# Kernel tuning notes

Measured on AMD Instinct MI355X. Metric: run time of the kernel, lower is better.

## Reference

```python
import jax, jax.numpy as jnp
import numpy as np

N_NODES = 50000
N_EDGES = 25000
NNZ = 600000
D = 128
H = 256
DEPTH = 2


def setup_inputs() -> dict:
    key = jax.random.key(0)
    ks = jax.random.split(key, 12)
    x = jax.random.normal(ks[0], (N_NODES, D), dtype=jnp.float32)
    v_idx = jax.random.randint(ks[1], (NNZ,), 0, N_NODES)
    e_idx = jax.random.randint(ks[2], (NNZ,), 0, N_EDGES)
    s = 0.05
    W1 = jax.random.normal(ks[3], (H, D), dtype=jnp.float32) * s
    b1 = jnp.zeros((H,), jnp.float32)
    W2 = jax.random.normal(ks[4], (D, H), dtype=jnp.float32) * s
    b2 = jnp.zeros((D,), jnp.float32)
    Wu = jax.random.normal(ks[5], (D, D), dtype=jnp.float32) * s
    bu = jnp.zeros((D,), jnp.float32)
    Wa = jax.random.normal(ks[6], (4, D), dtype=jnp.float32) * s
    ba = jnp.zeros((4,), jnp.float32)
    return {"x": x, "v_idx": v_idx, "e_idx": e_idx, "W1": W1, "b1": b1,
            "W2": W2, "b2": b2, "Wu": Wu, "bu": bu, "Wa": Wa, "ba": ba}


def reference(x, v_idx, e_idx, W1, b1, W2, b2, Wu, bu, Wa, ba):
    ones = jnp.ones((v_idx.shape[0],), x.dtype)
    # degrees for mean aggregation (clamped to avoid div-by-zero)
    edeg = jnp.maximum(jax.ops.segment_sum(ones, e_idx, num_segments=N_EDGES), 1.0)
    vdeg = jnp.maximum(jax.ops.segment_sum(ones, v_idx, num_segments=N_NODES), 1.0)

    def v2v_mean(m):
        # vertex -> hyperedge (mean), then hyperedge -> vertex (mean)
        e_feat = jax.ops.segment_sum(m[v_idx], e_idx, num_segments=N_EDGES) / edeg[:, None]
        return jax.ops.segment_sum(e_feat[e_idx], v_idx, num_segments=N_NODES) / vdeg[:, None]

    def update(h):
        m = jax.nn.relu(h @ W1.T + b1)   # [N, H]
        m = jax.nn.relu(m @ W2.T + b2)   # [N, D]  (dropout = identity in eval)
        m_i = v2v_mean(m)                # [N, D]
        return jax.nn.relu(h @ Wu.T + bu + m_i)

    for _ in range(DEPTH):
        x = update(x)
    a = x @ Wa.T + ba                    # [N, 4]
    return jax.nn.log_softmax(a, axis=1)
```

## Files before the change

kernel.cpp:

```cpp
#include <hip/hip_runtime.h>
#include <hip/hip_bf16.h>
#include <math.h>

#define N_NODES 50000
#define N_EDGES 25000
#define NNZ     600000
#define D       128
#define H       256

#define BW    98
#define NBE   256
#define NBV   511
#define CAPE  3072
#define CAPV  1536
#define CHUNK 4096

typedef short short8 __attribute__((ext_vector_type(8)));
typedef float floatx4 __attribute__((ext_vector_type(4)));

__device__ inline ushort f2bf(float f) {
    uint u = __float_as_uint(f);
    u += 0x7FFF + ((u >> 16) & 1);
    return (ushort)(u >> 16);
}
__device__ inline float bflo(uint u) { return __uint_as_float(u << 16); }
__device__ inline float bfhi(uint u) { return __uint_as_float(u & 0xffff0000u); }

__global__ void convert_all(const float* __restrict__ x,  ushort* __restrict__ xb,
                            const float* __restrict__ W1, ushort* __restrict__ W1b,
                            const float* __restrict__ W2, ushort* __restrict__ W2b,
                            const float* __restrict__ Wu, ushort* __restrict__ Wub) {
    const int nx = N_NODES * D / 4;
    const int n1 = H * D / 4;
    const int n2 = D * H / 4;
    const int nu = D * D / 4;
    int i = blockIdx.x * blockDim.x + threadIdx.x;
    const float* src; ushort* dst; int j = i;
    if (j < nx)                { src = x;  dst = xb;  }
    else if ((j -= nx) < n1)   { src = W1; dst = W1b; }
    else if ((j -= n1) < n2)   { src = W2; dst = W2b; }
    else if ((j -= n2) < nu)   { src = Wu; dst = Wub; }
    else return;
    float4 v = ((const float4*)src)[j];
    ushort4 o;
    o.x = f2bf(v.x); o.y = f2bf(v.y); o.z = f2bf(v.z); o.w = f2bf(v.w);
    ((ushort4*)dst)[j] = o;
}

__global__ void bucket_place(const int* __restrict__ v_idx, const int* __restrict__ e_idx,
                             int* __restrict__ cntE, int* __restrict__ cntV,
                             int2* __restrict__ recE, int2* __restrict__ recV) {
    __shared__ int hE[NBE], hV[NBV];
    __shared__ int rE[NBE], rV[NBV];
    for (int i = threadIdx.x; i < NBE; i += 256) hE[i] = 0;
    for (int i = threadIdx.x; i < NBV; i += 256) hV[i] = 0;
    __syncthreads();
    int base = blockIdx.x * CHUNK;
    int end  = min(base + CHUNK, NNZ);
    int myE[16], myV[16];
    #pragma unroll
    for (int j = 0; j < 16; ++j) {
        int i = base + threadIdx.x + j * 256;
        myE[j] = -1; myV[j] = -1;
        if (i < end) {
            myE[j] = e_idx[i];
            myV[j] = v_idx[i];
            atomicAdd(&hE[myE[j] / BW], 1);
            atomicAdd(&hV[myV[j] / BW], 1);
        }
    }
    __syncthreads();
    for (int i = threadIdx.x; i < NBE; i += 256) {
        int c = hE[i];
        rE[i] = c ? atomicAdd(&cntE[i], c) : 0;
    }
    for (int i = threadIdx.x; i < NBV; i += 256) {
        int c = hV[i];
        rV[i] = c ? atomicAdd(&cntV[i], c) : 0;
    }
    __syncthreads();
    for (int i = threadIdx.x; i < NBE; i += 256) hE[i] = 0;
    for (int i = threadIdx.x; i < NBV; i += 256) hV[i] = 0;
    __syncthreads();
    #pragma unroll
    for (int j = 0; j < 16; ++j) {
        if (myE[j] >= 0) {
            int bk = myE[j] / BW;
            int p = rE[bk] + atomicAdd(&hE[bk], 1);
            recE[(size_t)bk * CAPE + p] = make_int2(myE[j], myV[j]);
            bk = myV[j] / BW;
            p = rV[bk] + atomicAdd(&hV[bk], 1);
            recV[(size_t)bk * CAPV + p] = make_int2(myV[j], myE[j]);
        }
    }
}

__global__ void bucket_final(const int2* __restrict__ recE, const int* __restrict__ cntE,
                             const int2* __restrict__ recV, const int* __restrict__ cntV,
                             int2* __restrict__ e_sd, float* __restrict__ erecip, int* __restrict__ e_vert,
                             int2* __restrict__ v_sd, float* __restrict__ vrecip, int* __restrict__ v_edge) {
    __shared__ int hist[BW], scn[BW], cur[BW];
    const bool eSide = blockIdx.x < NBE;
    const int b = eSide ? blockIdx.x : blockIdx.x - NBE;
    const int cap   = eSide ? CAPE : CAPV;
    const int2* rec = (eSide ? recE : recV) + (size_t)b * cap;
    const int cnt   = (eSide ? cntE : cntV)[b];
    const int nseg  = eSide ? N_EDGES : N_NODES;
    int2* sd        = eSide ? e_sd : v_sd;
    float* recip    = eSide ? erecip : vrecip;
    int* outv       = (eSide ? e_vert : v_edge) + (size_t)b * cap;
    const int k0 = b * BW;

    for (int i = threadIdx.x; i < BW; i += 256) hist[i] = 0;
    __syncthreads();
    for (int i = threadIdx.x; i < cnt; i += 256)
        atomicAdd(&hist[rec[i].x - k0], 1);
    __syncthreads();

    if (threadIdx.x < 64) {
        int lane = threadIdx.x;
        int v0 = hist[lane];
        int a = v0;
        #pragma unroll
        for (int d = 1; d < 64; d <<= 1) {
            int u = __shfl_up(a, d, 64);
            if (lane >= d) a += u;
        }
        scn[lane] = a - v0;
        int tot0 = __shfl(a, 63, 64);
        int v1 = (lane < BW - 64) ? hist[64 + lane] : 0;
        int a1 = v1;
        #pragma unroll
        for (int d = 1; d < 64; d <<= 1) {
            int u = __shfl_up(a1, d, 64);
            if (lane >= d) a1 += u;
        }
        if (lane < BW - 64) scn[64 + lane] = tot0 + a1 - v1;
    }
    __syncthreads();

    const int gbase = b * cap;
    for (int i = threadIdx.x; i < BW; i += 256) {
        int seg = k0 + i;
        if (seg < nseg) {
            sd[seg] = make_int2(gbase + scn[i], hist[i]);
            recip[seg] = 1.0f / (float)max(hist[i], 1);
        }
        cur[i] = scn[i];
    }
    __syncthreads();
    for (int i = threadIdx.x; i < cnt; i += 256) {
        int2 r = rec[i];
        int p = atomicAdd(&cur[r.x - k0], 1);
        outv[p] = r.y;
    }
}

__global__ void gather_rows(const ushort* __restrict__ src,
                            const int2* __restrict__ sd,
                            const int* __restrict__ list,
                            const float* __restrict__ recip,
                            const ushort* __restrict__ uadd,
                            ushort* __restrict__ outbuf,
                            const float* __restrict__ Wa,
                            const float* __restrict__ ba,
                            float* __restrict__ headout,
                            int nseg) {
    long long gtid = (long long)blockIdx.x * blockDim.x + threadIdx.x;
    int seg = (int)(gtid >> 4);
    int ql  = threadIdx.x & 15;
    if (seg >= nseg) return;
    int2 dsc = sd[seg];
    int s = dsc.x, cnt = dsc.y;
    const ushort* sp = src + ql * 8;

    float f0 = 0.f, f1 = 0.f, f2 = 0.f, f3 = 0.f;
    float f4 = 0.f, f5 = 0.f, f6 = 0.f, f7 = 0.f;

    int p = 0;
    for (; p + 4 <= cnt; p += 4) {
        int r0 = list[s + p + 0];
        int r1 = list[s + p + 1];
        int r2 = list[s + p + 2];
        int r3 = list[s + p + 3];
        uint4 t0 = *(const uint4*)(sp + (size_t)r0 * D);
        uint4 t1 = *(const uint4*)(sp + (size_t)r1 * D);
        uint4 t2 = *(const uint4*)(sp + (size_t)r2 * D);
        uint4 t3 = *(const uint4*)(sp + (size_t)r3 * D);
        f0 += bflo(t0.x) + bflo(t1.x) + bflo(t2.x) + bflo(t3.x);
        f1 += bfhi(t0.x) + bfhi(t1.x) + bfhi(t2.x) + bfhi(t3.x);
        f2 += bflo(t0.y) + bflo(t1.y) + bflo(t2.y) + bflo(t3.y);
        f3 += bfhi(t0.y) + bfhi(t1.y) + bfhi(t2.y) + bfhi(t3.y);
        f4 += bflo(t0.z) + bflo(t1.z) + bflo(t2.z) + bflo(t3.z);
        f5 += bfhi(t0.z) + bfhi(t1.z) + bfhi(t2.z) + bfhi(t3.z);
        f6 += bflo(t0.w) + bflo(t1.w) + bflo(t2.w) + bflo(t3.w);
        f7 += bfhi(t0.w) + bfhi(t1.w) + bfhi(t2.w) + bfhi(t3.w);
    }
    for (; p < cnt; ++p) {
        int r0 = list[s + p];
        uint4 t0 = *(const uint4*)(sp + (size_t)r0 * D);
        f0 += bflo(t0.x);  f1 += bfhi(t0.x);
        f2 += bflo(t0.y);  f3 += bfhi(t0.y);
        f4 += bflo(t0.z);  f5 += bfhi(t0.z);
        f6 += bflo(t0.w);  f7 += bfhi(t0.w);
    }

    float rc = recip[seg];
    f0 *= rc; f1 *= rc; f2 *= rc; f3 *= rc;
    f4 *= rc; f5 *= rc; f6 *= rc; f7 *= rc;
    if (uadd) {
        uint4 uv = *(const uint4*)(uadd + (size_t)seg * D + ql * 8);
        f0 = fmaxf(f0 + bflo(uv.x), 0.f);  f1 = fmaxf(f1 + bfhi(uv.x), 0.f);
        f2 = fmaxf(f2 + bflo(uv.y), 0.f);  f3 = fmaxf(f3 + bfhi(uv.y), 0.f);
        f4 = fmaxf(f4 + bflo(uv.z), 0.f);  f5 = fmaxf(f5 + bfhi(uv.z), 0.f);
        f6 = fmaxf(f6 + bflo(uv.w), 0.f);  f7 = fmaxf(f7 + bfhi(uv.w), 0.f);
    }
    if (headout) {
        float av[4];
        #pragma unroll
        for (int j = 0; j < 4; ++j) {
            const float* wr = Wa + j * D + ql * 8;
            float4 wA = *(const float4*)wr;
            float4 wB = *(const float4*)(wr + 4);
            float pj = f0 * wA.x + f1 * wA.y + f2 * wA.z + f3 * wA.w
                     + f4 * wB.x + f5 * wB.y + f6 * wB.z + f7 * wB.w;
            pj += __shfl_xor(pj, 1, 64);
            pj += __shfl_xor(pj, 2, 64);
            pj += __shfl_xor(pj, 4, 64);
            pj += __shfl_xor(pj, 8, 64);
            av[j] = pj + ba[j];
        }
        if (ql == 0) {
            float mx = fmaxf(fmaxf(av[0], av[1]), fmaxf(av[2], av[3]));
            float se = expf(av[0] - mx) + expf(av[1] - mx)
                     + expf(av[2] - mx) + expf(av[3] - mx);
            float lse = mx + logf(se);
            float4 o = make_float4(av[0] - lse, av[1] - lse, av[2] - lse, av[3] - lse);
            *(float4*)(headout + (size_t)seg * 4) = o;
        }
    } else {
        uint4 o;
        o.x = ((uint)f2bf(f1) << 16) | (uint)f2bf(f0);
        o.y = ((uint)f2bf(f3) << 16) | (uint)f2bf(f2);
        o.z = ((uint)f2bf(f5) << 16) | (uint)f2bf(f4);
        o.w = ((uint)f2bf(f7) << 16) | (uint)f2bf(f6);
        *(uint4*)(outbuf + (size_t)seg * D + ql * 8) = o;
    }
}

__launch_bounds__(256, 3)
__global__ void mlp_fused(const ushort* __restrict__ A,
                          const ushort* __restrict__ W1b,
                          const float* __restrict__ b1,
                          const ushort* __restrict__ W2b,
                          const float* __restrict__ b2,
                          const ushort* __restrict__ Wub,
                          const float* __restrict__ bu,
                          ushort* __restrict__ m2out,
                          ushort* __restrict__ uout,
                          int M) {
    __shared__ ushort Af[64][136];
    __shared__ __align__(16) char Pbuf[18432];
    __shared__ ushort m1c[64][72];
    ushort* P = (ushort*)Pbuf;
    float (*Cs)[68] = (float(*)[68])Pbuf;

    const int tid = threadIdx.x;
    const int w = tid >> 6, lane = tid & 63;
    const int quad = lane >> 4, mrow = lane & 15;
    const int rowBase = blockIdx.x * 64;
    const int orow = tid >> 2;
    const int c0   = (tid & 3) << 4;

    #pragma unroll
    for (int r = 0; r < 4; ++r) {
        int idx = tid + r * 256;
        int row = idx >> 4;
        int c   = (idx & 15) << 3;
        uint4 av = make_uint4(0, 0, 0, 0);
        if (rowBase + row < M)
            av = *(const uint4*)(A + (size_t)(rowBase + row) * D + c);
        *(uint4*)&Af[row][c] = av;
    }

    for (int n0 = 0; n0 < D; n0 += 64) {
        __syncthreads();
        #pragma unroll
        for (int r = 0; r < 4; ++r) {
            int idx = tid + r * 256;
            int row = idx >> 4;
            int c   = (idx & 15) << 3;
            *(uint4*)&P[row * 136 + c] = *(const uint4*)(Wub + (size_t)(n0 + row) * D + c);
        }
        __syncthreads();
        floatx4 acc[4] = {{0,0,0,0},{0,0,0,0},{0,0,0,0},{0,0,0,0}};
        #pragma unroll
        for (int k0 = 0; k0 < D; k0 += 32) {
            short8 af = *(const short8*)&Af[w * 16 + mrow][k0 + quad * 8];
            #pragma unroll
            for (int t = 0; t < 4; ++t) {
                short8 bfr = *(const short8*)&P[(t * 16 + mrow) * 136 + k0 + quad * 8];
                acc[t] = __builtin_amdgcn_mfma_f32_16x16x32_bf16(af, bfr, acc[t], 0, 0, 0);
            }
        }
        __syncthreads();
        #pragma unroll
        for (int t = 0; t < 4; ++t)
            #pragma unroll
            for (int r = 0; r < 4; ++r)
                Cs[w * 16 + quad * 4 + r][t * 16 + mrow] = acc[t][r];
        __syncthreads();
        if (rowBase + orow < M) {
            union { ushort u16[16]; uint4 u4[2]; } ov;
            #pragma unroll
            for (int j4 = 0; j4 < 4; ++j4) {
                float4 bb = *(const float4*)(bu + n0 + c0 + j4 * 4);
                float bjv[4] = {bb.x, bb.y, bb.z, bb.w};
                #pragma unroll
                for (int j = 0; j < 4; ++j)
                    ov.u16[j4 * 4 + j] = f2bf(Cs[orow][c0 + j4 * 4 + j] + bjv[j]);
            }
            ushort* cp = uout + (size_t)(rowBase + orow) * D + n0 + c0;
            *(uint4*)cp = ov.u4[0];
            *(uint4*)(cp + 8) = ov.u4[1];
        }
    }

    floatx4 acc2[8] = {{0,0,0,0},{0,0,0,0},{0,0,0,0},{0,0,0,0},
                       {0,0,0,0},{0,0,0,0},{0,0,0,0},{0,0,0,0}};
    for (int kc = 0; kc < 4; ++kc) {
        __syncthreads();
        #pragma unroll
        for (int r = 0; r < 4; ++r) {
            int idx = tid + r * 256;
            int row = idx >> 4;
            int c   = (idx & 15) << 3;
            *(uint4*)&P[row * 136 + c] = *(const uint4*)(W1b + (size_t)(kc * 64 + row) * D + c);
        }
        __syncthreads();
        floatx4 acc1[4] = {{0,0,0,0},{0,0,0,0},{0,0,0,0},{0,0,0,0}};
        #pragma unroll
        for (int k0 = 0; k0 < D; k0 += 32) {
            short8 af = *(const short8*)&Af[w * 16 + mrow][k0 + quad * 8];
            #pragma unroll
            for (int t = 0; t < 4; ++t) {
                short8 bfr = *(const short8*)&P[(t * 16 + mrow) * 136 + k0 + quad * 8];
                acc1[t] = __builtin_amdgcn_mfma_f32_16x16x32_bf16(af, bfr, acc1[t], 0, 0, 0);
            }
        }
        #pragma unroll
        for (int t = 0; t < 4; ++t) {
            float bb = b1[kc * 64 + t * 16 + mrow];
            #pragma unroll
            for (int r = 0; r < 4; ++r)
                m1c[w * 16 + quad * 4 + r][t * 16 + mrow] = f2bf(fmaxf(acc1[t][r] + bb, 0.f));
        }
        __syncthreads();
        #pragma unroll
        for (int r = 0; r < 4; ++r) {
            int idx = tid + r * 256;
            int row = idx >> 3;
            int c8  = (idx & 7) << 3;
            *(uint4*)&P[row * 72 + c8] = *(const uint4*)(W2b + (size_t)row * H + kc * 64 + c8);
        }
        __syncthreads();
        #pragma unroll
        for (int k0 = 0; k0 < 64; k0 += 32) {
            short8 af = *(const short8*)&m1c[w * 16 + mrow][k0 + quad * 8];
            #pragma unroll
            for (int t2 = 0; t2 < 8; ++t2) {
                short8 bfr = *(const short8*)&P[(t2 * 16 + mrow) * 72 + k0 + quad * 8];
                acc2[t2] = __builtin_amdgcn_mfma_f32_16x16x32_bf16(af, bfr, acc2[t2], 0, 0, 0);
            }
        }
    }

    #pragma unroll
    for (int hh = 0; hh < 2; ++hh) {
        __syncthreads();
        #pragma unroll
        for (int t = 0; t < 4; ++t)
            #pragma unroll
            for (int r = 0; r < 4; ++r)
                Cs[w * 16 + quad * 4 + r][t * 16 + mrow] = acc2[hh * 4 + t][r];
        __syncthreads();
        if (rowBase + orow < M) {
            union { ushort u16[16]; uint4 u4[2]; } ov;
            #pragma unroll
            for (int j4 = 0; j4 < 4; ++j4) {
                float4 bb = *(const float4*)(b2 + hh * 64 + c0 + j4 * 4);
                float bjv[4] = {bb.x, bb.y, bb.z, bb.w};
                #pragma unroll
                for (int j = 0; j < 4; ++j) {
                    float v = Cs[orow][c0 + j4 * 4 + j] + bjv[j];
                    ov.u16[j4 * 4 + j] = f2bf(fmaxf(v, 0.f));
                }
            }
            ushort* cp = m2out + (size_t)(rowBase + orow) * D + hh * 64 + c0;
            *(uint4*)cp = ov.u4[0];
            *(uint4*)(cp + 8) = ov.u4[1];
        }
    }
}

extern "C" void kernel_launch(void* const* d_in, const int* in_sizes, int n_in,
                              void* d_out, int out_size, void* d_ws, size_t ws_size,
                              hipStream_t stream) {
    const float* x     = (const float*)d_in[0];
    const int*   v_idx = (const int*)d_in[1];
    const int*   e_idx = (const int*)d_in[2];
    const float* W1    = (const float*)d_in[3];
    const float* b1    = (const float*)d_in[4];
    const float* W2    = (const float*)d_in[5];
    const float* b2    = (const float*)d_in[6];
    const float* Wu    = (const float*)d_in[7];
    const float* bu    = (const float*)d_in[8];
    const float* Wa    = (const float*)d_in[9];
    const float* ba    = (const float*)d_in[10];
    float* out = (float*)d_out;

    char* wsp = (char*)d_ws;
    auto alloc = [&](size_t bytes) -> char* {
        char* p = wsp;
        wsp += (bytes + 255) & ~(size_t)255;
        return p;
    };

    ushort* xb     = (ushort*)alloc((size_t)N_NODES * D * 2);
    ushort* hA     = (ushort*)alloc((size_t)N_NODES * D * 2);
    ushort* m2b    = (ushort*)alloc((size_t)N_NODES * D * 2);
    ushort* ub     = (ushort*)alloc((size_t)N_NODES * D * 2);
    ushort* e_feat = (ushort*)alloc((size_t)N_EDGES * D * 2);
    ushort* W1b    = (ushort*)alloc((size_t)H * D * 2);
    ushort* W2b    = (ushort*)alloc((size_t)D * H * 2);
    ushort* Wub    = (ushort*)alloc((size_t)D * D * 2);
    int*    e_vert = (int*)alloc((size_t)NBE * CAPE * 4);
    int*    v_edge = (int*)alloc((size_t)NBV * CAPV * 4);
    int2*   recE   = (int2*)alloc((size_t)NBE * CAPE * 8);
    int2*   recV   = (int2*)alloc((size_t)NBV * CAPV * 8);
    int*    cntE   = (int*)alloc((size_t)(NBE + NBV) * 4);
    int*    cntV   = cntE + NBE;
    int2*   e_sd   = (int2*)alloc((size_t)N_EDGES * 8);
    int2*   v_sd   = (int2*)alloc((size_t)N_NODES * 8);
    float*  erecip = (float*)alloc((size_t)N_EDGES * 4);
    float*  vrecip = (float*)alloc((size_t)N_NODES * 4);

    const int cooBlocks = (NNZ + CHUNK - 1) / CHUNK;
    const int convTotal = N_NODES * D / 4 + H * D / 4 + D * H / 4 + D * D / 4;

    convert_all<<<(convTotal + 255) / 256, 256, 0, stream>>>(
        x, xb, W1, W1b, W2, W2b, Wu, Wub);

    hipMemsetAsync(cntE, 0, (size_t)(NBE + NBV) * 4, stream);
    bucket_place<<<cooBlocks, 256, 0, stream>>>(v_idx, e_idx, cntE, cntV, recE, recV);
    bucket_final<<<NBE + NBV, 256, 0, stream>>>(recE, cntE, recV, cntV,
                                                e_sd, erecip, e_vert,
                                                v_sd, vrecip, v_edge);

    const int gridM = (N_NODES + 63) / 64;
    const int gEdge = (N_EDGES * 16 + 255) / 256;
    const int gVert = (N_NODES * 16 + 255) / 256;

    const ushort* h = xb;
    for (int depth = 0; depth < 2; ++depth) {
        mlp_fused<<<gridM, 256, 0, stream>>>(h, W1b, b1, W2b, b2, Wub, bu, m2b, ub, N_NODES);
        gather_rows<<<gEdge, 256, 0, stream>>>(
            m2b, e_sd, e_vert, erecip, nullptr, e_feat, nullptr, nullptr, nullptr, N_EDGES);
        if (depth == 0) {
            gather_rows<<<gVert, 256, 0, stream>>>(
                e_feat, v_sd, v_edge, vrecip, ub, hA, nullptr, nullptr, nullptr, N_NODES);
            h = hA;
        } else {
            gather_rows<<<gVert, 256, 0, stream>>>(
                e_feat, v_sd, v_edge, vrecip, ub, nullptr, Wa, ba, out, N_NODES);
        }
    }
}
```

Measured before the change: 269.6 us.

## Fuse input fp32-to-bf16 conversion into MLP and double rows per block

Drops the separate conversion pass over x: the first-depth MLP kernel now reads fp32 rows directly and converts them to bf16 while staging into shared memory. This removes one full write and read of a bf16 copy of x. The MLP block tile also grows from 64 to 128 rows, with two row groups sharing each loaded weight tile, which halves weight staging per row. In exchange it uses more LDS and accumulator registers, and occupancy drops to two blocks per CU.

```diff
diff --git a/kernel.cpp b/kernel.cpp
--- a/kernel.cpp
+++ b/kernel.cpp
@@ -26,18 +26,15 @@
 __device__ inline float bflo(uint u) { return __uint_as_float(u << 16); }
 __device__ inline float bfhi(uint u) { return __uint_as_float(u & 0xffff0000u); }
 
-__global__ void convert_all(const float* __restrict__ x,  ushort* __restrict__ xb,
-                            const float* __restrict__ W1, ushort* __restrict__ W1b,
-                            const float* __restrict__ W2, ushort* __restrict__ W2b,
-                            const float* __restrict__ Wu, ushort* __restrict__ Wub) {
-    const int nx = N_NODES * D / 4;
+__global__ void convert_weights(const float* __restrict__ W1, ushort* __restrict__ W1b,
+                                const float* __restrict__ W2, ushort* __restrict__ W2b,
+                                const float* __restrict__ Wu, ushort* __restrict__ Wub) {
     const int n1 = H * D / 4;
     const int n2 = D * H / 4;
     const int nu = D * D / 4;
-    int i = blockIdx.x * blockDim.x + threadIdx.x;
-    const float* src; ushort* dst; int j = i;
-    if (j < nx)                { src = x;  dst = xb;  }
-    else if ((j -= nx) < n1)   { src = W1; dst = W1b; }
+    int j = blockIdx.x * blockDim.x + threadIdx.x;
+    const float* src; ushort* dst;
+    if (j < n1)                { src = W1; dst = W1b; }
     else if ((j -= n1) < n2)   { src = W2; dst = W2b; }
     else if ((j -= n2) < nu)   { src = Wu; dst = Wub; }
     else return;
@@ -248,8 +245,8 @@
     }
 }
 
-__launch_bounds__(256, 3)
-__global__ void mlp_fused(const ushort* __restrict__ A,
+__launch_bounds__(256, 2)
+__global__ void mlp_fused(const void* __restrict__ Aptr, int a_fp32,
                           const ushort* __restrict__ W1b,
                           const float* __restrict__ b1,
                           const ushort* __restrict__ W2b,
@@ -259,27 +256,39 @@
                           ushort* __restrict__ m2out,
                           ushort* __restrict__ uout,
                           int M) {
-    __shared__ ushort Af[64][136];
+    __shared__ ushort Af[128][136];
     __shared__ __align__(16) char Pbuf[18432];
-    __shared__ ushort m1c[64][72];
+    __shared__ __align__(16) char UB[18432];
     ushort* P = (ushort*)Pbuf;
-    float (*Cs)[68] = (float(*)[68])Pbuf;
+    ushort (*m1c)[72] = (ushort(*)[72])UB;
+    float (*Cs)[68] = (float(*)[68])UB;
 
     const int tid = threadIdx.x;
     const int w = tid >> 6, lane = tid & 63;
     const int quad = lane >> 4, mrow = lane & 15;
-    const int rowBase = blockIdx.x * 64;
+    const int rowBase = blockIdx.x * 128;
     const int orow = tid >> 2;
     const int c0   = (tid & 3) << 4;
 
     #pragma unroll
-    for (int r = 0; r < 4; ++r) {
+    for (int r = 0; r < 8; ++r) {
         int idx = tid + r * 256;
         int row = idx >> 4;
         int c   = (idx & 15) << 3;
         uint4 av = make_uint4(0, 0, 0, 0);
-        if (rowBase + row < M)
-            av = *(const uint4*)(A + (size_t)(rowBase + row) * D + c);
+        if (rowBase + row < M) {
+            if (a_fp32) {
+                const float* ap = (const float*)Aptr + (size_t)(rowBase + row) * D + c;
+                float4 va = *(const float4*)ap;
+                float4 vb = *(const float4*)(ap + 4);
+                av.x = ((uint)f2bf(va.y) << 16) | (uint)f2bf(va.x);
+                av.y = ((uint)f2bf(va.w) << 16) | (uint)f2bf(va.z);
+                av.z = ((uint)f2bf(vb.y) << 16) | (uint)f2bf(vb.x);
+                av.w = ((uint)f2bf(vb.w) << 16) | (uint)f2bf(vb.z);
+            } else {
+                av = *(const uint4*)((const ushort*)Aptr + (size_t)(rowBase + row) * D + c);
+            }
+        }
         *(uint4*)&Af[row][c] = av;
     }
 
@@ -293,41 +302,46 @@
             *(uint4*)&P[row * 136 + c] = *(const uint4*)(Wub + (size_t)(n0 + row) * D + c);
         }
         __syncthreads();
-        floatx4 acc[4] = {{0,0,0,0},{0,0,0,0},{0,0,0,0},{0,0,0,0}};
-        #pragma unroll
-        for (int k0 = 0; k0 < D; k0 += 32) {
-            short8 af = *(const short8*)&Af[w * 16 + mrow][k0 + quad * 8];
+        #pragma unroll
+        for (int rg = 0; rg < 2; ++rg) {
+            floatx4 acc[4] = {{0,0,0,0},{0,0,0,0},{0,0,0,0},{0,0,0,0}};
             #pragma unroll
-            for (int t = 0; t < 4; ++t) {
-                short8 bfr = *(const short8*)&P[(t * 16 + mrow) * 136 + k0 + quad * 8];
-                acc[t] = __builtin_amdgcn_mfma_f32_16x16x32_bf16(af, bfr, acc[t], 0, 0, 0);
-            }
-        }
-        __syncthreads();
-        #pragma unroll
-        for (int t = 0; t < 4; ++t)
+            for (int k0 = 0; k0 < D; k0 += 32) {
+                short8 af = *(const short8*)&Af[rg * 64 + w * 16 + mrow][k0 + quad * 8];
+                #pragma unroll
+                for (int t = 0; t < 4; ++t) {
+                    short8 bfr = *(const short8*)&P[(t * 16 + mrow) * 136 + k0 + quad * 8];
+                    acc[t] = __builtin_amdgcn_mfma_f32_16x16x32_bf16(af, bfr, acc[t], 0, 0, 0);
+                }
+            }
+            __syncthreads();
             #pragma unroll
-            for (int r = 0; r < 4; ++r)
-                Cs[w * 16 + quad * 4 + r][t * 16 + mrow] = acc[t][r];
-        __syncthreads();
-        if (rowBase + orow < M) {
-            union { ushort u16[16]; uint4 u4[2]; } ov;
-            #pragma unroll
-            for (int j4 = 0; j4 < 4; ++j4) {
-                float4 bb = *(const float4*)(bu + n0 + c0 + j4 * 4);
-                float bjv[4] = {bb.x, bb.y, bb.z, bb.w};
-                #pragma unroll
-                for (int j = 0; j < 4; ++j)
-                    ov.u16[j4 * 4 + j] = f2bf(Cs[orow][c0 + j4 * 4 + j] + bjv[j]);
-            }
-            ushort* cp = uout + (size_t)(rowBase + orow) * D + n0 + c0;
-            *(uint4*)cp = ov.u4[0];
-            *(uint4*)(cp + 8) = ov.u4[1];
-        }
-    }
-
-    floatx4 acc2[8] = {{0,0,0,0},{0,0,0,0},{0,0,0,0},{0,0,0,0},
-                       {0,0,0,0},{0,0,0,0},{0,0,0,0},{0,0,0,0}};
+            for (int t = 0; t < 4; ++t)
+                #pragma unroll
+                for (int r = 0; r < 4; ++r)
+                    Cs[w * 16 + quad * 4 + r][t * 16 + mrow] = acc[t][r];
+            __syncthreads();
+            int grow = rowBase + rg * 64 + orow;
+            if (grow < M) {
+                union { ushort u16[16]; uint4 u4[2]; } ov;
+                #pragma unroll
+                for (int j4 = 0; j4 < 4; ++j4) {
+                    float4 cv = *(const float4*)&Cs[orow][c0 + j4 * 4];
+                    float4 bb = *(const float4*)(bu + n0 + c0 + j4 * 4);
+                    ov.u16[j4 * 4 + 0] = f2bf(cv.x + bb.x);
+                    ov.u16[j4 * 4 + 1] = f2bf(cv.y + bb.y);
+                    ov.u16[j4 * 4 + 2] = f2bf(cv.z + bb.z);
+                    ov.u16[j4 * 4 + 3] = f2bf(cv.w + bb.w);
+                }
+                ushort* cp = uout + (size_t)grow * D + n0 + c0;
+                *(uint4*)cp = ov.u4[0];
+                *(uint4*)(cp + 8) = ov.u4[1];
+            }
+            __syncthreads();
+        }
+    }
+
+    floatx4 acc2[2][8] = {};
     for (int kc = 0; kc < 4; ++kc) {
         __syncthreads();
         #pragma unroll
@@ -338,22 +352,26 @@
             *(uint4*)&P[row * 136 + c] = *(const uint4*)(W1b + (size_t)(kc * 64 + row) * D + c);
         }
         __syncthreads();
-        floatx4 acc1[4] = {{0,0,0,0},{0,0,0,0},{0,0,0,0},{0,0,0,0}};
-        #pragma unroll
-        for (int k0 = 0; k0 < D; k0 += 32) {
-            short8 af = *(const short8*)&Af[w * 16 + mrow][k0 + quad * 8];
+        #pragma unroll
+        for (int rg = 0; rg < 2; ++rg) {
+            floatx4 acc1[4] = {{0,0,0,0},{0,0,0,0},{0,0,0,0},{0,0,0,0}};
+            #pragma unroll
+            for (int k0 = 0; k0 < D; k0 += 32) {
+                short8 af = *(const short8*)&Af[rg * 64 + w * 16 + mrow][k0 + quad * 8];
+                #pragma unroll
+                for (int t = 0; t < 4; ++t) {
+                    short8 bfr = *(const short8*)&P[(t * 16 + mrow) * 136 + k0 + quad * 8];
+                    acc1[t] = __builtin_amdgcn_mfma_f32_16x16x32_bf16(af, bfr, acc1[t], 0, 0, 0);
+                }
+            }
             #pragma unroll
             for (int t = 0; t < 4; ++t) {
-                short8 bfr = *(const short8*)&P[(t * 16 + mrow) * 136 + k0 + quad * 8];
-                acc1[t] = __builtin_amdgcn_mfma_f32_16x16x32_bf16(af, bfr, acc1[t], 0, 0, 0);
-            }
-        }
-        #pragma unroll
-        for (int t = 0; t < 4; ++t) {
-            float bb = b1[kc * 64 + t * 16 + mrow];
-            #pragma unroll
-            for (int r = 0; r < 4; ++r)
-                m1c[w * 16 + quad * 4 + r][t * 16 + mrow] = f2bf(fmaxf(acc1[t][r] + bb, 0.f));
+                float bb = b1[kc * 64 + t * 16 + mrow];
+                #pragma unroll
+                for (int r = 0; r < 4; ++r)
+                    m1c[rg * 64 + w * 16 + quad * 4 + r][t * 16 + mrow] =
+                        f2bf(fmaxf(acc1[t][r] + bb, 0.f));
+            }
         }
         __syncthreads();
         #pragma unroll
@@ -365,40 +383,46 @@
         }
         __syncthreads();
         #pragma unroll
-        for (int k0 = 0; k0 < 64; k0 += 32) {
-            short8 af = *(const short8*)&m1c[w * 16 + mrow][k0 + quad * 8];
+        for (int rg = 0; rg < 2; ++rg) {
             #pragma unroll
-            for (int t2 = 0; t2 < 8; ++t2) {
-                short8 bfr = *(const short8*)&P[(t2 * 16 + mrow) * 72 + k0 + quad * 8];
-                acc2[t2] = __builtin_amdgcn_mfma_f32_16x16x32_bf16(af, bfr, acc2[t2], 0, 0, 0);
+            for (int k0 = 0; k0 < 64; k0 += 32) {
+                short8 af = *(const short8*)&m1c[rg * 64 + w * 16 + mrow][k0 + quad * 8];
+                #pragma unroll
+                for (int t2 = 0; t2 < 8; ++t2) {
+                    short8 bfr = *(const short8*)&P[(t2 * 16 + mrow) * 72 + k0 + quad * 8];
+                    acc2[rg][t2] = __builtin_amdgcn_mfma_f32_16x16x32_bf16(af, bfr, acc2[rg][t2], 0, 0, 0);
+                }
             }
         }
     }
 
     #pragma unroll
-    for (int hh = 0; hh < 2; ++hh) {
-        __syncthreads();
-        #pragma unroll
-        for (int t = 0; t < 4; ++t)
+    for (int rg = 0; rg < 2; ++rg) {
+        #pragma unroll
+        for (int hh = 0; hh < 2; ++hh) {
+            __syncthreads();
             #pragma unroll
-            for (int r = 0; r < 4; ++r)
-                Cs[w * 16 + quad * 4 + r][t * 16 + mrow] = acc2[hh * 4 + t][r];
-        __syncthreads();
-        if (rowBase + orow < M) {
-            union { ushort u16[16]; uint4 u4[2]; } ov;
-            #pragma unroll
-            for (int j4 = 0; j4 < 4; ++j4) {
-                float4 bb = *(const float4*)(b2 + hh * 64 + c0 + j4 * 4);
-                float bjv[4] = {bb.x, bb.y, bb.z, bb.w};
-                #pragma unroll
-                for (int j = 0; j < 4; ++j) {
-                    float v = Cs[orow][c0 + j4 * 4 + j] + bjv[j];
-                    ov.u16[j4 * 4 + j] = f2bf(fmaxf(v, 0.f));
+            for (int t = 0; t < 4; ++t)
+                #pragma unroll
+                for (int r = 0; r < 4; ++r)
+                    Cs[w * 16 + quad * 4 + r][t * 16 + mrow] = acc2[rg][hh * 4 + t][r];
+            __syncthreads();
+            int grow = rowBase + rg * 64 + orow;
+            if (grow < M) {
+                union { ushort u16[16]; uint4 u4[2]; } ov;
+                #pragma unroll
+                for (int j4 = 0; j4 < 4; ++j4) {
+                    float4 cv = *(const float4*)&Cs[orow][c0 + j4 * 4];
+                    float4 bb = *(const float4*)(b2 + hh * 64 + c0 + j4 * 4);
+                    ov.u16[j4 * 4 + 0] = f2bf(fmaxf(cv.x + bb.x, 0.f));
+                    ov.u16[j4 * 4 + 1] = f2bf(fmaxf(cv.y + bb.y, 0.f));
+                    ov.u16[j4 * 4 + 2] = f2bf(fmaxf(cv.z + bb.z, 0.f));
+                    ov.u16[j4 * 4 + 3] = f2bf(fmaxf(cv.w + bb.w, 0.f));
                 }
-            }
-            ushort* cp = m2out + (size_t)(rowBase + orow) * D + hh * 64 + c0;
-            *(uint4*)cp = ov.u4[0];
-            *(uint4*)(cp + 8) = ov.u4[1];
+                ushort* cp = m2out + (size_t)grow * D + hh * 64 + c0;
+                *(uint4*)cp = ov.u4[0];
+                *(uint4*)(cp + 8) = ov.u4[1];
+            }
         }
     }
 }
@@ -426,7 +450,6 @@
         return p;
     };
 
-    ushort* xb     = (ushort*)alloc((size_t)N_NODES * D * 2);
     ushort* hA     = (ushort*)alloc((size_t)N_NODES * D * 2);
     ushort* m2b    = (ushort*)alloc((size_t)N_NODES * D * 2);
     ushort* ub     = (ushort*)alloc((size_t)N_NODES * D * 2);
@@ -446,10 +469,10 @@
     float*  vrecip = (float*)alloc((size_t)N_NODES * 4);
 
     const int cooBlocks = (NNZ + CHUNK - 1) / CHUNK;
-    const int convTotal = N_NODES * D / 4 + H * D / 4 + D * H / 4 + D * D / 4;
-
-    convert_all<<<(convTotal + 255) / 256, 256, 0, stream>>>(
-        x, xb, W1, W1b, W2, W2b, Wu, Wub);
+    const int convTotal = H * D / 4 + D * H / 4 + D * D / 4;
+
+    convert_weights<<<(convTotal + 255) / 256, 256, 0, stream>>>(
+        W1, W1b, W2, W2b, Wu, Wub);
 
     hipMemsetAsync(cntE, 0, (size_t)(NBE + NBV) * 4, stream);
     bucket_place<<<cooBlocks, 256, 0, stream>>>(v_idx, e_idx, cntE, cntV, recE, recV);
@@ -457,19 +480,22 @@
                                                 e_sd, erecip, e_vert,
                                                 v_sd, vrecip, v_edge);
 
-    const int gridM = (N_NODES + 63) / 64;
+    const int gridM = (N_NODES + 127) / 128;
     const int gEdge = (N_EDGES * 16 + 255) / 256;
     const int gVert = (N_NODES * 16 + 255) / 256;
 
-    const ushort* h = xb;
+    const void* h = x;
+    int h_fp32 = 1;
     for (int depth = 0; depth < 2; ++depth) {
-        mlp_fused<<<gridM, 256, 0, stream>>>(h, W1b, b1, W2b, b2, Wub, bu, m2b, ub, N_NODES);
+        mlp_fused<<<gridM, 256, 0, stream>>>(h, h_fp32, W1b, b1, W2b, b2, Wub, bu,
+                                             m2b, ub, N_NODES);
         gather_rows<<<gEdge, 256, 0, stream>>>(
             m2b, e_sd, e_vert, erecip, nullptr, e_feat, nullptr, nullptr, nullptr, N_EDGES);
         if (depth == 0) {
             gather_rows<<<gVert, 256, 0, stream>>>(
                 e_feat, v_sd, v_edge, vrecip, ub, hA, nullptr, nullptr, nullptr, N_NODES);
             h = hA;
+            h_fp32 = 0;
         } else {
             gather_rows<<<gVert, 256, 0, stream>>>(
                 e_feat, v_sd, v_edge, vrecip, ub, nullptr, Wa, ba, out, N_NODES);
```

Result: faster. 260.9 us (-3.2%).

## Restructure MLP kernel to per-wave tiles with direct weight loads, fuse x conversion

Applied to the files above, without the earlier changes.

The fused MLP kernel is rewritten so each wave owns an independent 16-row tile, keeps its A fragments in registers, and reads weight fragments straight from global/L2 instead of staging them through shared memory behind block-wide barriers. The fp32 input x is converted to bf16 inside the first MLP launch, which removes the separate full-tensor conversion pass. The weight conversion is merged into the bucket placement kernel to cut one launch. Outputs are now written as scattered 2-byte stores instead of vectorized rows, and weight reads rely on cache hits, which may add memory traffic.

```diff
diff --git a/kernel.cpp b/kernel.cpp
--- a/kernel.cpp
+++ b/kernel.cpp
@@ -26,36 +26,42 @@
 __device__ inline float bflo(uint u) { return __uint_as_float(u << 16); }
 __device__ inline float bfhi(uint u) { return __uint_as_float(u & 0xffff0000u); }
 
-__global__ void convert_all(const float* __restrict__ x,  ushort* __restrict__ xb,
-                            const float* __restrict__ W1, ushort* __restrict__ W1b,
-                            const float* __restrict__ W2, ushort* __restrict__ W2b,
-                            const float* __restrict__ Wu, ushort* __restrict__ Wub) {
-    const int nx = N_NODES * D / 4;
-    const int n1 = H * D / 4;
-    const int n2 = D * H / 4;
-    const int nu = D * D / 4;
-    int i = blockIdx.x * blockDim.x + threadIdx.x;
-    const float* src; ushort* dst; int j = i;
-    if (j < nx)                { src = x;  dst = xb;  }
-    else if ((j -= nx) < n1)   { src = W1; dst = W1b; }
-    else if ((j -= n1) < n2)   { src = W2; dst = W2b; }
-    else if ((j -= n2) < nu)   { src = Wu; dst = Wub; }
-    else return;
-    float4 v = ((const float4*)src)[j];
-    ushort4 o;
-    o.x = f2bf(v.x); o.y = f2bf(v.y); o.z = f2bf(v.z); o.w = f2bf(v.w);
-    ((ushort4*)dst)[j] = o;
-}
-
-__global__ void bucket_place(const int* __restrict__ v_idx, const int* __restrict__ e_idx,
-                             int* __restrict__ cntE, int* __restrict__ cntV,
-                             int2* __restrict__ recE, int2* __restrict__ recV) {
+__device__ inline short8 ldg8(const ushort* p) {
+    union { uint4 u4; short8 s8; } cv;
+    cv.u4 = *(const uint4*)p;
+    return cv.s8;
+}
+
+__global__ void convert_and_place(const float* __restrict__ W1, ushort* __restrict__ W1b,
+                                  const float* __restrict__ W2, ushort* __restrict__ W2b,
+                                  const float* __restrict__ Wu, ushort* __restrict__ Wub,
+                                  const int* __restrict__ v_idx, const int* __restrict__ e_idx,
+                                  int* __restrict__ cntE, int* __restrict__ cntV,
+                                  int2* __restrict__ recE, int2* __restrict__ recV,
+                                  int convBlocks) {
+    if ((int)blockIdx.x < convBlocks) {
+        const int n1 = H * D / 4;
+        const int n2 = D * H / 4;
+        const int nu = D * D / 4;
+        int j = blockIdx.x * 256 + threadIdx.x;
+        const float* src; ushort* dst;
+        if (j < n1)                { src = W1; dst = W1b; }
+        else if ((j -= n1) < n2)   { src = W2; dst = W2b; }
+        else if ((j -= n2) < nu)   { src = Wu; dst = Wub; }
+        else return;
+        float4 v = ((const float4*)src)[j];
+        ushort4 o;
+        o.x = f2bf(v.x); o.y = f2bf(v.y); o.z = f2bf(v.z); o.w = f2bf(v.w);
+        ((ushort4*)dst)[j] = o;
+        return;
+    }
+
     __shared__ int hE[NBE], hV[NBV];
     __shared__ int rE[NBE], rV[NBV];
     for (int i = threadIdx.x; i < NBE; i += 256) hE[i] = 0;
     for (int i = threadIdx.x; i < NBV; i += 256) hV[i] = 0;
     __syncthreads();
-    int base = blockIdx.x * CHUNK;
+    int base = (blockIdx.x - convBlocks) * CHUNK;
     int end  = min(base + CHUNK, NNZ);
     int myE[16], myV[16];
     #pragma unroll
@@ -248,8 +254,8 @@
     }
 }
 
-__launch_bounds__(256, 3)
-__global__ void mlp_fused(const ushort* __restrict__ A,
+__launch_bounds__(256, 4)
+__global__ void mlp_fused(const void* __restrict__ Aptr, int a_fp32,
                           const ushort* __restrict__ W1b,
                           const float* __restrict__ b1,
                           const ushort* __restrict__ W2b,
@@ -259,146 +265,90 @@
                           ushort* __restrict__ m2out,
                           ushort* __restrict__ uout,
                           int M) {
-    __shared__ ushort Af[64][136];
-    __shared__ __align__(16) char Pbuf[18432];
-    __shared__ ushort m1c[64][72];
-    ushort* P = (ushort*)Pbuf;
-    float (*Cs)[68] = (float(*)[68])Pbuf;
+    __shared__ ushort m1s[4][16][264];
 
     const int tid = threadIdx.x;
     const int w = tid >> 6, lane = tid & 63;
     const int quad = lane >> 4, mrow = lane & 15;
-    const int rowBase = blockIdx.x * 64;
-    const int orow = tid >> 2;
-    const int c0   = (tid & 3) << 4;
-
-    #pragma unroll
-    for (int r = 0; r < 4; ++r) {
-        int idx = tid + r * 256;
-        int row = idx >> 4;
-        int c   = (idx & 15) << 3;
-        uint4 av = make_uint4(0, 0, 0, 0);
-        if (rowBase + row < M)
-            av = *(const uint4*)(A + (size_t)(rowBase + row) * D + c);
-        *(uint4*)&Af[row][c] = av;
-    }
-
-    for (int n0 = 0; n0 < D; n0 += 64) {
-        __syncthreads();
+    const int tileId = blockIdx.x * 4 + w;
+    const int row0 = tileId * 16;
+    const bool active = row0 < M;
+
+    short8 afr[4];
+
+    if (active) {
+        if (a_fp32) {
+            const float* ap = (const float*)Aptr + (size_t)(row0 + mrow) * D + quad * 8;
+            #pragma unroll
+            for (int ks = 0; ks < 4; ++ks) {
+                float4 va = *(const float4*)(ap + ks * 32);
+                float4 vb = *(const float4*)(ap + ks * 32 + 4);
+                union { ushort us[8]; short8 s8; } cv;
+                cv.us[0] = f2bf(va.x); cv.us[1] = f2bf(va.y);
+                cv.us[2] = f2bf(va.z); cv.us[3] = f2bf(va.w);
+                cv.us[4] = f2bf(vb.x); cv.us[5] = f2bf(vb.y);
+                cv.us[6] = f2bf(vb.z); cv.us[7] = f2bf(vb.w);
+                afr[ks] = cv.s8;
+            }
+        } else {
+            const ushort* ap = (const ushort*)Aptr + (size_t)(row0 + mrow) * D + quad * 8;
+            #pragma unroll
+            for (int ks = 0; ks < 4; ++ks)
+                afr[ks] = ldg8(ap + ks * 32);
+        }
+
+        const ushort* w1p = W1b + (size_t)mrow * D + quad * 8;
+        #pragma unroll 2
+        for (int t = 0; t < 16; ++t) {
+            floatx4 acc = {0.f, 0.f, 0.f, 0.f};
+            #pragma unroll
+            for (int ks = 0; ks < 4; ++ks) {
+                short8 wf = ldg8(w1p + (size_t)t * 16 * D + ks * 32);
+                acc = __builtin_amdgcn_mfma_f32_16x16x32_bf16(afr[ks], wf, acc, 0, 0, 0);
+            }
+            float bb = b1[t * 16 + mrow];
+            #pragma unroll
+            for (int r = 0; r < 4; ++r)
+                m1s[w][quad * 4 + r][t * 16 + mrow] = f2bf(fmaxf(acc[r] + bb, 0.f));
+        }
+
+        const ushort* wup = Wub + (size_t)mrow * D + quad * 8;
+        #pragma unroll 2
+        for (int t = 0; t < 8; ++t) {
+            floatx4 acc = {0.f, 0.f, 0.f, 0.f};
+            #pragma unroll
+            for (int ks = 0; ks < 4; ++ks) {
+                short8 wf = ldg8(wup + (size_t)t * 16 * D + ks * 32);
+                acc = __builtin_amdgcn_mfma_f32_16x16x32_bf16(afr[ks], wf, acc, 0, 0, 0);
+            }
+            float bb = bu[t * 16 + mrow];
+            #pragma unroll
+            for (int r = 0; r < 4; ++r)
+                uout[(size_t)(row0 + quad * 4 + r) * D + t * 16 + mrow] = f2bf(acc[r] + bb);
+        }
+    }
+
+    __syncthreads();
+
+    if (active) {
+        floatx4 acc2[8] = {};
+        const ushort* w2p = W2b + (size_t)mrow * H + quad * 8;
         #pragma unroll
-        for (int r = 0; r < 4; ++r) {
-            int idx = tid + r * 256;
-            int row = idx >> 4;
-            int c   = (idx & 15) << 3;
-            *(uint4*)&P[row * 136 + c] = *(const uint4*)(Wub + (size_t)(n0 + row) * D + c);
-        }
-        __syncthreads();
-        floatx4 acc[4] = {{0,0,0,0},{0,0,0,0},{0,0,0,0},{0,0,0,0}};
+        for (int ks = 0; ks < 8; ++ks) {
+            short8 af = *(const short8*)&m1s[w][mrow][ks * 32 + quad * 8];
+            #pragma unroll
+            for (int t = 0; t < 8; ++t) {
+                short8 wf = ldg8(w2p + (size_t)t * 16 * H + ks * 32);
+                acc2[t] = __builtin_amdgcn_mfma_f32_16x16x32_bf16(af, wf, acc2[t], 0, 0, 0);
+            }
+        }
         #pragma unroll
-        for (int k0 = 0; k0 < D; k0 += 32) {
-            short8 af = *(const short8*)&Af[w * 16 + mrow][k0 + quad * 8];
-            #pragma unroll
-            for (int t = 0; t < 4; ++t) {
-                short8 bfr = *(const short8*)&P[(t * 16 + mrow) * 136 + k0 + quad * 8];
-                acc[t] = __builtin_amdgcn_mfma_f32_16x16x32_bf16(af, bfr, acc[t], 0, 0, 0);
-            }
-        }
-        __syncthreads();
-        #pragma unroll
-        for (int t = 0; t < 4; ++t)
+        for (int t = 0; t < 8; ++t) {
+            float bb = b2[t * 16 + mrow];
             #pragma unroll
             for (int r = 0; r < 4; ++r)
-                Cs[w * 16 + quad * 4 + r][t * 16 + mrow] = acc[t][r];
-        __syncthreads();
-        if (rowBase + orow < M) {
-            union { ushort u16[16]; uint4 u4[2]; } ov;
-            #pragma unroll
-            for (int j4 = 0; j4 < 4; ++j4) {
-                float4 bb = *(const float4*)(bu + n0 + c0 + j4 * 4);
-                float bjv[4] = {bb.x, bb.y, bb.z, bb.w};
-                #pragma unroll
-                for (int j = 0; j < 4; ++j)
-                    ov.u16[j4 * 4 + j] = f2bf(Cs[orow][c0 + j4 * 4 + j] + bjv[j]);
-            }
-            ushort* cp = uout + (size_t)(rowBase + orow) * D + n0 + c0;
-            *(uint4*)cp = ov.u4[0];
-            *(uint4*)(cp + 8) = ov.u4[1];
-        }
-    }
-
-    floatx4 acc2[8] = {{0,0,0,0},{0,0,0,0},{0,0,0,0},{0,0,0,0},
-                       {0,0,0,0},{0,0,0,0},{0,0,0,0},{0,0,0,0}};
-    for (int kc = 0; kc < 4; ++kc) {
-        __syncthreads();
-        #pragma unroll
-        for (int r = 0; r < 4; ++r) {
-            int idx = tid + r * 256;
-            int row = idx >> 4;
-            int c   = (idx & 15) << 3;
-            *(uint4*)&P[row * 136 + c] = *(const uint4*)(W1b + (size_t)(kc * 64 + row) * D + c);
-        }
-        __syncthreads();
-        floatx4 acc1[4] = {{0,0,0,0},{0,0,0,0},{0,0,0,0},{0,0,0,0}};
-        #pragma unroll
-        for (int k0 = 0; k0 < D; k0 += 32) {
-            short8 af = *(const short8*)&Af[w * 16 + mrow][k0 + quad * 8];
-            #pragma unroll
-            for (int t = 0; t < 4; ++t) {
-                short8 bfr = *(const short8*)&P[(t * 16 + mrow) * 136 + k0 + quad * 8];
-                acc1[t] = __builtin_amdgcn_mfma_f32_16x16x32_bf16(af, bfr, acc1[t], 0, 0, 0);
-            }
-        }
-        #pragma unroll
-        for (int t = 0; t < 4; ++t) {
-            float bb = b1[kc * 64 + t * 16 + mrow];
-            #pragma unroll
-            for (int r = 0; r < 4; ++r)
-                m1c[w * 16 + quad * 4 + r][t * 16 + mrow] = f2bf(fmaxf(acc1[t][r] + bb, 0.f));
-        }
-        __syncthreads();
-        #pragma unroll
-        for (int r = 0; r < 4; ++r) {
-            int idx = tid + r * 256;
-            int row = idx >> 3;
-            int c8  = (idx & 7) << 3;
-            *(uint4*)&P[row * 72 + c8] = *(const uint4*)(W2b + (size_t)row * H + kc * 64 + c8);
-        }
-        __syncthreads();
-        #pragma unroll
-        for (int k0 = 0; k0 < 64; k0 += 32) {
-            short8 af = *(const short8*)&m1c[w * 16 + mrow][k0 + quad * 8];
-            #pragma unroll
-            for (int t2 = 0; t2 < 8; ++t2) {
-                short8 bfr = *(const short8*)&P[(t2 * 16 + mrow) * 72 + k0 + quad * 8];
-                acc2[t2] = __builtin_amdgcn_mfma_f32_16x16x32_bf16(af, bfr, acc2[t2], 0, 0, 0);
-            }
-        }
-    }
-
-    #pragma unroll
-    for (int hh = 0; hh < 2; ++hh) {
-        __syncthreads();
-        #pragma unroll
-        for (int t = 0; t < 4; ++t)
-            #pragma unroll
-            for (int r = 0; r < 4; ++r)
-                Cs[w * 16 + quad * 4 + r][t * 16 + mrow] = acc2[hh * 4 + t][r];
-        __syncthreads();
-        if (rowBase + orow < M) {
-            union { ushort u16[16]; uint4 u4[2]; } ov;
-            #pragma unroll
-            for (int j4 = 0; j4 < 4; ++j4) {
-                float4 bb = *(const float4*)(b2 + hh * 64 + c0 + j4 * 4);
-                float bjv[4] = {bb.x, bb.y, bb.z, bb.w};
-                #pragma unroll
-                for (int j = 0; j < 4; ++j) {
-                    float v = Cs[orow][c0 + j4 * 4 + j] + bjv[j];
-                    ov.u16[j4 * 4 + j] = f2bf(fmaxf(v, 0.f));
-                }
-            }
-            ushort* cp = m2out + (size_t)(rowBase + orow) * D + hh * 64 + c0;
-            *(uint4*)cp = ov.u4[0];
-            *(uint4*)(cp + 8) = ov.u4[1];
+                m2out[(size_t)(row0 + quad * 4 + r) * D + t * 16 + mrow] =
+                    f2bf(fmaxf(acc2[t][r] + bb, 0.f));
         }
     }
 }
@@ -426,7 +376,6 @@
         return p;
     };
 
-    ushort* xb     = (ushort*)alloc((size_t)N_NODES * D * 2);
     ushort* hA     = (ushort*)alloc((size_t)N_NODES * D * 2);
     ushort* m2b    = (ushort*)alloc((size_t)N_NODES * D * 2);
     ushort* ub     = (ushort*)alloc((size_t)N_NODES * D * 2);
@@ -445,31 +394,34 @@
     float*  erecip = (float*)alloc((size_t)N_EDGES * 4);
     float*  vrecip = (float*)alloc((size_t)N_NODES * 4);
 
-    const int cooBlocks = (NNZ + CHUNK - 1) / CHUNK;
-    const int convTotal = N_NODES * D / 4 + H * D / 4 + D * H / 4 + D * D / 4;
-
-    convert_all<<<(convTotal + 255) / 256, 256, 0, stream>>>(
-        x, xb, W1, W1b, W2, W2b, Wu, Wub);
+    const int cooBlocks  = (NNZ + CHUNK - 1) / CHUNK;
+    const int convTotal  = H * D / 4 + D * H / 4 + D * D / 4;
+    const int convBlocks = (convTotal + 255) / 256;
 
     hipMemsetAsync(cntE, 0, (size_t)(NBE + NBV) * 4, stream);
-    bucket_place<<<cooBlocks, 256, 0, stream>>>(v_idx, e_idx, cntE, cntV, recE, recV);
+    convert_and_place<<<convBlocks + cooBlocks, 256, 0, stream>>>(
+        W1, W1b, W2, W2b, Wu, Wub, v_idx, e_idx, cntE, cntV, recE, recV, convBlocks);
     bucket_final<<<NBE + NBV, 256, 0, stream>>>(recE, cntE, recV, cntV,
                                                 e_sd, erecip, e_vert,
                                                 v_sd, vrecip, v_edge);
 
-    const int gridM = (N_NODES + 63) / 64;
-    const int gEdge = (N_EDGES * 16 + 255) / 256;
-    const int gVert = (N_NODES * 16 + 255) / 256;
-
-    const ushort* h = xb;
+    const int nTiles = N_NODES / 16;
+    const int gridM  = (nTiles + 3) / 4;
+    const int gEdge  = (N_EDGES * 16 + 255) / 256;
+    const int gVert  = (N_NODES * 16 + 255) / 256;
+
+    const void* h = x;
+    int h_fp32 = 1;
     for (int depth = 0; depth < 2; ++depth) {
-        mlp_fused<<<gridM, 256, 0, stream>>>(h, W1b, b1, W2b, b2, Wub, bu, m2b, ub, N_NODES);
+        mlp_fused<<<gridM, 256, 0, stream>>>(h, h_fp32, W1b, b1, W2b, b2, Wub, bu,
+                                             m2b, ub, N_NODES);
         gather_rows<<<gEdge, 256, 0, stream>>>(
             m2b, e_sd, e_vert, erecip, nullptr, e_feat, nullptr, nullptr, nullptr, N_EDGES);
         if (depth == 0) {
             gather_rows<<<gVert, 256, 0, stream>>>(
                 e_feat, v_sd, v_edge, vrecip, ub, hA, nullptr, nullptr, nullptr, N_NODES);
             h = hA;
+            h_fp32 = 0;
         } else {
             gather_rows<<<gVert, 256, 0, stream>>>(
                 e_feat, v_sd, v_edge, vrecip, ub, nullptr, Wa, ba, out, N_NODES);
```

After: 370.0 us. 1.37x slower.
